# Optimization experiments

Measured on AMD Instinct MI355X. Metric: run time of the kernel, lower is better.

The kernel has to match this reference:

```python
import jax, jax.numpy as jnp
import numpy as np

B, N, D_IN, D_OUT = 4, 2048, 1024, 1024


def setup_inputs() -> dict:
    key = jax.random.key(0)
    k0, k1, k2, k3 = jax.random.split(key, 4)
    x = jax.random.normal(k0, (B, N, D_IN), dtype=jnp.float32)
    # torch Linear weight is [out, in]; store transposed [in, out] for x @ W
    W_query = jax.random.normal(k1, (D_IN, D_OUT), dtype=jnp.float32) * (D_IN ** -0.5)
    W_key = jax.random.normal(k2, (D_IN, D_OUT), dtype=jnp.float32) * (D_IN ** -0.5)
    W_value = jax.random.normal(k3, (D_IN, D_OUT), dtype=jnp.float32) * (D_IN ** -0.5)
    return {"x": x, "W_query": W_query, "W_key": W_key, "W_value": W_value}


def reference(x, W_query, W_key, W_value):
    # x: [B, N, D_IN]
    num_tokens = x.shape[1]
    embed_dim = x.shape[2]  # NB: original scales by INPUT embed dim
    q = jnp.einsum('bnd,de->bne', x, W_query)  # [B, N, D_OUT]
    k = jnp.einsum('bnd,de->bne', x, W_key)
    v = jnp.einsum('bnd,de->bne', x, W_value)
    scores = jnp.einsum('bqe,bke->bqk', q, k)  # [B, N, N]
    idx = jnp.arange(num_tokens)
    causal_mask = idx[None, :] > idx[:, None]  # True above diagonal
    scores = jnp.where(causal_mask[None, :, :], -jnp.inf, scores)
    scale = jnp.asarray(embed_dim, scores.dtype) ** 0.5
    attn = jax.nn.softmax(scores / scale, axis=-1)  # dropout p=0 (eval)
    context = jnp.einsum('bqk,bke->bqe', attn, v)  # [B, N, D_OUT]
    return context
```

## Files before the change

kernel.cpp:

```cpp
#include <hip/hip_runtime.h>


typedef __attribute__((ext_vector_type(8))) _Float16 half8;
typedef __attribute__((ext_vector_type(4))) _Float16 half4v;
typedef __attribute__((ext_vector_type(4))) float floatx4;

#define AS1 __attribute__((address_space(1)))
#define AS3 __attribute__((address_space(3)))

__device__ __forceinline__ void load16_lds(void* lds, const void* g) {
  __builtin_amdgcn_global_load_lds((AS1 void*)g, (AS3 void*)lds, 16, 0, 0);
}

__global__ __launch_bounds__(256)
void prep(const float* __restrict__ in, _Float16* __restrict__ out,
          const float* __restrict__ W0, const float* __restrict__ W1,
          const float* __restrict__ W2, _Float16* __restrict__ Wt) {
  const int bid = blockIdx.x;
  if (bid < 8192) {
    const int i = (bid * 256 + threadIdx.x) << 2;
    float4 v = *(const float4*)(in + i);
    half4v o = { (_Float16)v.x, (_Float16)v.y, (_Float16)v.z, (_Float16)v.w };
    *(half4v*)(out + i) = o;
  } else {
    const int t = bid - 8192;
    const int bz = t >> 10;
    const int rem = t & 1023;
    const int bx = rem & 31, by = rem >> 5;
    const float* W = bz == 0 ? W0 : (bz == 1 ? W1 : W2);
    _Float16* o = Wt + (long long)bz * 1048576;
    __shared__ _Float16 tl[32][33];
    const int tx = threadIdx.x & 31, ty = threadIdx.x >> 5;
    const int n0 = bx << 5, k0 = by << 5;
#pragma unroll
    for (int i = 0; i < 4; ++i)
      tl[ty + i * 8][tx] = (_Float16)W[(long long)(k0 + ty + i * 8) * 1024 + n0 + tx];
    __syncthreads();
#pragma unroll
    for (int i = 0; i < 4; ++i)
      o[(long long)(n0 + ty + i * 8) * 1024 + k0 + tx] = tl[tx][ty + i * 8];
  }
}

__global__ __launch_bounds__(256)
void gemm_qkv(const _Float16* __restrict__ A, const _Float16* __restrict__ B,
              _Float16* __restrict__ Q, _Float16* __restrict__ Kh,
              _Float16* __restrict__ Vt) {
  const int bm = blockIdx.y, bn = blockIdx.x;
  const _Float16* Ab = A + (long long)bm * 128 * 1024;
  const _Float16* Bb = B + (long long)bn * 128 * 1024;

  __shared__ _Float16 As[128][64];
  __shared__ _Float16 Bs[128][64];

  const int tid = threadIdx.x;
  const int wave = tid >> 6, lane = tid & 63;
  const int quad = lane >> 4, lr = lane & 15;
  const int wm = (wave >> 1) << 6, wn = (wave & 1) << 6;
  const int srow = lane >> 3;
  const int goff = ((lane & 7) ^ srow) << 3;

  floatx4 acc[4][4] = {};
  const _Float16* ga = Ab + (long long)(wave * 8 + srow) * 1024 + goff;
  const _Float16* gb = Bb + (long long)(wave * 8 + srow) * 1024 + goff;

  for (int k0 = 0; k0 < 1024; k0 += 64) {
    __syncthreads();
#pragma unroll
    for (int c = 0; c < 4; ++c) {
      load16_lds(&As[wave * 8 + 32 * c][0], ga + c * 32 * 1024);
      load16_lds(&Bs[wave * 8 + 32 * c][0], gb + c * 32 * 1024);
    }
    ga += 64; gb += 64;
    __syncthreads();

#pragma unroll
    for (int kk = 0; kk < 2; ++kk) {
      half8 af[4], bf[4];
#pragma unroll
      for (int i = 0; i < 4; ++i) {
        const int ra = wm + (i << 4) + lr;
        const int rb = wn + (i << 4) + lr;
        af[i] = *(const half8*)&As[ra][(((kk << 2) + quad) ^ (ra & 7)) << 3];
        bf[i] = *(const half8*)&Bs[rb][(((kk << 2) + quad) ^ (rb & 7)) << 3];
      }
#pragma unroll
      for (int i = 0; i < 4; ++i)
#pragma unroll
        for (int j = 0; j < 4; ++j)
          acc[i][j] = __builtin_amdgcn_mfma_f32_16x16x32_f16(af[i], bf[j], acc[i][j], 0, 0, 0);
    }
  }

  const int colb = bn * 128 + wn + lr;
  const int rowb = bm * 128 + wm + (quad << 2);

  if (bn < 16) {
    _Float16* C = (bn < 8) ? Q : Kh;
    const int cb = colb & 1023;
#pragma unroll
    for (int i = 0; i < 4; ++i)
#pragma unroll
      for (int j = 0; j < 4; ++j)
#pragma unroll
        for (int r = 0; r < 4; ++r)
          C[(long long)(rowb + (i << 4) + r) * 1024 + cb + (j << 4)] =
              (_Float16)acc[i][j][r];
  } else {
    const int b = rowb >> 11;
    const int tb = rowb & 2047;
#pragma unroll
    for (int i = 0; i < 4; ++i) {
      const int tok = tb + (i << 4);
#pragma unroll
      for (int j = 0; j < 4; ++j) {
        const int d = (colb & 1023) + (j << 4);
        half4v v = { (_Float16)acc[i][j][0], (_Float16)acc[i][j][1],
                     (_Float16)acc[i][j][2], (_Float16)acc[i][j][3] };
        *(half4v*)&Vt[(long long)b * 2097152 + (long long)d * 2048 + tok] = v;
      }
    }
  }
}

__global__ __launch_bounds__(256)
void gemm_s_exp(const _Float16* __restrict__ Q, const _Float16* __restrict__ Kh,
                _Float16* __restrict__ P, float* __restrict__ M,
                float* __restrict__ L) {
  int t = (blockIdx.x & 7) * 34 + (blockIdx.x >> 3);
  int bn = 0;
  for (;;) { const int c = 32 - 2 * bn; if (t < c) break; t -= c; ++bn; }
  const int qm = 2 * bn + t;
  const int bz = blockIdx.y;

  const _Float16* Ab = Q  + (long long)bz * 2097152 + (long long)qm * 64 * 1024;
  const _Float16* Bb = Kh + (long long)bz * 2097152 + (long long)bn * 128 * 1024;

  __shared__ _Float16 As[64][64];
  __shared__ _Float16 Bs[128][64];
  __shared__ float sm_m[2][2][32];
  __shared__ float sm_s[2][2][32];

  const int tid = threadIdx.x;
  const int wave = tid >> 6, lane = tid & 63;
  const int quad = lane >> 4, lr = lane & 15;
  const int wm1 = wave >> 1, wn1 = wave & 1;
  const int wm = wm1 << 5, wn = wn1 << 6;
  const int srow = lane >> 3;
  const int schunk = lane & 7;
  const int goff = (schunk ^ srow) << 3;

  floatx4 acc[2][4] = {};
  const _Float16* ga = Ab + (long long)(wave * 8 + srow) * 1024 + goff;
  const _Float16* gb = Bb + (long long)(wave * 8 + srow) * 1024 + goff;

  half8 pa[2], pb[4];
#pragma unroll
  for (int c = 0; c < 2; ++c) pa[c] = *(const half8*)(ga + c * 32 * 1024);
#pragma unroll
  for (int c = 0; c < 4; ++c) pb[c] = *(const half8*)(gb + c * 32 * 1024);

  for (int it = 0; it < 16; ++it) {
    __syncthreads();
#pragma unroll
    for (int c = 0; c < 2; ++c)
      *(half8*)&As[wave * 8 + 32 * c + srow][schunk << 3] = pa[c];
#pragma unroll
    for (int c = 0; c < 4; ++c)
      *(half8*)&Bs[wave * 8 + 32 * c + srow][schunk << 3] = pb[c];
    __syncthreads();
    if (it + 1 < 16) {
      const int k1 = (it + 1) << 6;
#pragma unroll
      for (int c = 0; c < 2; ++c)
        pa[c] = *(const half8*)(ga + c * 32 * 1024 + k1);
#pragma unroll
      for (int c = 0; c < 4; ++c)
        pb[c] = *(const half8*)(gb + c * 32 * 1024 + k1);
    }

#pragma unroll
    for (int kk = 0; kk < 2; ++kk) {
      half8 af[2], bf[4];
#pragma unroll
      for (int i = 0; i < 2; ++i) {
        const int ra = wm + (i << 4) + lr;
        af[i] = *(const half8*)&As[ra][(((kk << 2) + quad) ^ (ra & 7)) << 3];
      }
#pragma unroll
      for (int j = 0; j < 4; ++j) {
        const int rb = wn + (j << 4) + lr;
        bf[j] = *(const half8*)&Bs[rb][(((kk << 2) + quad) ^ (rb & 7)) << 3];
      }
#pragma unroll
      for (int i = 0; i < 2; ++i)
#pragma unroll
        for (int j = 0; j < 4; ++j)
          acc[i][j] = __builtin_amdgcn_mfma_f32_16x16x32_f16(af[i], bf[j], acc[i][j], 0, 0, 0);
    }
  }

  const int colb = bn * 128 + wn + lr;
  const int rowb = qm * 64 + wm + (quad << 2);
  _Float16* Pb = P + (long long)bz * 4194304;
  const float scl = 0.03125f;

  float mx[2][4], rs[2][4];
#pragma unroll
  for (int i = 0; i < 2; ++i)
#pragma unroll
    for (int r = 0; r < 4; ++r) { mx[i][r] = -3.0e38f; rs[i][r] = 0.f; }

#pragma unroll
  for (int i = 0; i < 2; ++i)
#pragma unroll
    for (int j = 0; j < 4; ++j)
#pragma unroll
      for (int r = 0; r < 4; ++r) {
        const int qr = rowb + (i << 4) + r;
        const int kcol = colb + (j << 4);
        if (kcol <= qr) mx[i][r] = fmaxf(mx[i][r], acc[i][j][r] * scl);
      }
#pragma unroll
  for (int i = 0; i < 2; ++i)
#pragma unroll
    for (int r = 0; r < 4; ++r) {
#pragma unroll
      for (int off = 1; off < 16; off <<= 1)
        mx[i][r] = fmaxf(mx[i][r], __shfl_xor(mx[i][r], off));
    }

  if (lr == 0) {
#pragma unroll
    for (int i = 0; i < 2; ++i)
#pragma unroll
      for (int r = 0; r < 4; ++r)
        sm_m[wm1][wn1][(i << 4) + (quad << 2) + r] = mx[i][r];
  }
  __syncthreads();
  float mt[2][4];
#pragma unroll
  for (int i = 0; i < 2; ++i)
#pragma unroll
    for (int r = 0; r < 4; ++r)
      mt[i][r] = fmaxf(mx[i][r], sm_m[wm1][wn1 ^ 1][(i << 4) + (quad << 2) + r]);

#pragma unroll
  for (int i = 0; i < 2; ++i)
#pragma unroll
    for (int j = 0; j < 4; ++j)
#pragma unroll
      for (int r = 0; r < 4; ++r) {
        const int qr = rowb + (i << 4) + r;
        const int kcol = colb + (j << 4);
        const float pv =
            (kcol <= qr) ? __expf(acc[i][j][r] * scl - mt[i][r]) : 0.f;
        Pb[(long long)qr * 2048 + kcol] = (_Float16)pv;
        rs[i][r] += pv;
      }

#pragma unroll
  for (int i = 0; i < 2; ++i)
#pragma unroll
    for (int r = 0; r < 4; ++r) {
#pragma unroll
      for (int off = 1; off < 16; off <<= 1)
        rs[i][r] += __shfl_xor(rs[i][r], off);
    }

  if (lr == 0) {
#pragma unroll
    for (int i = 0; i < 2; ++i)
#pragma unroll
      for (int r = 0; r < 4; ++r)
        sm_s[wm1][wn1][(i << 4) + (quad << 2) + r] = rs[i][r];
  }
  __syncthreads();
  if (wn1 == 0 && lr == 0) {
    float* Mb = M + ((long long)bz * 16 + bn) * 2048;
    float* Lb = L + ((long long)bz * 16 + bn) * 2048;
#pragma unroll
    for (int i = 0; i < 2; ++i)
#pragma unroll
      for (int r = 0; r < 4; ++r) {
        const int lrow = (i << 4) + (quad << 2) + r;
        const int row = rowb + (i << 4) + r;
        Mb[row] = mt[i][r];
        Lb[row] = rs[i][r] + sm_s[wm1][1][lrow];
      }
  }
}

__global__ __launch_bounds__(256)
void gemm_pv(const _Float16* __restrict__ P, const _Float16* __restrict__ Vt,
             const float* __restrict__ M, const float* __restrict__ L,
             float* __restrict__ out) {
  const int lid = blockIdx.x + (blockIdx.y << 3) + (blockIdx.z << 7);
  const int xcd = lid & 7;
  const int s = lid >> 3;
  const int p = s >> 4;
  const int dnl = (s >> 2) & 3;
  const int bz = s & 3;
  const int bmg = xcd >> 1, dng = xcd & 1;
  const int bm = (p < 2) ? (15 - 2 * bmg - p) : (2 * bmg + (3 - p));
  const int dn = dng * 4 + dnl;
  const int niter = 2 * (bm + 1);

  const _Float16* Ab = Vt + (long long)bz * 2097152 + (long long)dn * 128 * 2048;
  const _Float16* Bb = P  + (long long)bz * 4194304 + (long long)bm * 128 * 2048;

  __shared__ _Float16 As[128][64];
  __shared__ _Float16 Bs[128][64];
  __shared__ float F_lds[16][128];
  __shared__ float linv_lds[128];

  const int tid = threadIdx.x;
  const int wave = tid >> 6, lane = tid & 63;
  const int quad = lane >> 4, lr = lane & 15;
  const int wm = (wave >> 1) << 6, wn = (wave & 1) << 6;
  const int srow = lane >> 3;
  const int schunk = lane & 7;
  const int goff = (schunk ^ srow) << 3;
  const int lrow0 = wave * 8 + srow;

  if (tid < 128) {
    const float* Mb = M + (long long)bz * 32768 + bm * 128 + tid;
    const float* Lb = L + (long long)bz * 32768 + bm * 128 + tid;
    float mg = -3.0e38f;
    for (int t = 0; t <= bm; ++t) mg = fmaxf(mg, Mb[t * 2048]);
    float ssum = 0.f;
    for (int t = 0; t <= bm; ++t) {
      const float f = __expf(Mb[t * 2048] - mg);
      F_lds[t][tid] = f;
      ssum += f * Lb[t * 2048];
    }
    linv_lds[tid] = 1.0f / ssum;
  }

  floatx4 acc[4][4] = {};
  const _Float16* ga = Ab + (long long)lrow0 * 2048 + goff;
  const _Float16* gb = Bb + (long long)lrow0 * 2048 + goff;

  half8 pa[4], pb[4];
#pragma unroll
  for (int c = 0; c < 4; ++c) {
    pa[c] = *(const half8*)(ga + (long long)c * 32 * 2048);
    pb[c] = *(const half8*)(gb + (long long)c * 32 * 2048);
  }

  for (int it = 0; it < niter; ++it) {
    __syncthreads();
    const int kt = it >> 1;
#pragma unroll
    for (int c = 0; c < 4; ++c) {
      *(half8*)&As[wave * 8 + 32 * c + srow][schunk << 3] = pa[c];
      *(half8*)&Bs[wave * 8 + 32 * c + srow][schunk << 3] =
          pb[c] * (_Float16)F_lds[kt][lrow0 + 32 * c];
    }
    __syncthreads();
    if (it + 1 < niter) {
      const int k1 = (it + 1) << 6;
#pragma unroll
      for (int c = 0; c < 4; ++c) {
        pa[c] = *(const half8*)(ga + (long long)c * 32 * 2048 + k1);
        pb[c] = *(const half8*)(gb + (long long)c * 32 * 2048 + k1);
      }
    }

#pragma unroll
    for (int kk = 0; kk < 2; ++kk) {
      half8 af[4], bf[4];
#pragma unroll
      for (int i = 0; i < 4; ++i) {
        const int ra = wm + (i << 4) + lr;
        const int rb = wn + (i << 4) + lr;
        af[i] = *(const half8*)&As[ra][(((kk << 2) + quad) ^ (ra & 7)) << 3];
        bf[i] = *(const half8*)&Bs[rb][(((kk << 2) + quad) ^ (rb & 7)) << 3];
      }
#pragma unroll
      for (int i = 0; i < 4; ++i)
#pragma unroll
        for (int j = 0; j < 4; ++j)
          acc[i][j] = __builtin_amdgcn_mfma_f32_16x16x32_f16(af[i], bf[j], acc[i][j], 0, 0, 0);
    }
  }

  float* Cb = out + (long long)bz * 2097152;
  const int d0 = dn * 128 + wm + (quad << 2);
  const int q0 = bm * 128 + wn + lr;

  float linv[4];
#pragma unroll
  for (int j = 0; j < 4; ++j) linv[j] = linv_lds[wn + (j << 4) + lr];

#pragma unroll
  for (int i = 0; i < 4; ++i)
#pragma unroll
    for (int j = 0; j < 4; ++j) {
      float4 v = { acc[i][j][0] * linv[j], acc[i][j][1] * linv[j],
                   acc[i][j][2] * linv[j], acc[i][j][3] * linv[j] };
      *(float4*)&Cb[(long long)(q0 + (j << 4)) * 1024 + d0 + (i << 4)] = v;
    }
}


extern "C" void kernel_launch(void* const* d_in, const int* in_sizes, int n_in,
                              void* d_out, int out_size, void* d_ws, size_t ws_size,
                              hipStream_t stream) {
  const float* x  = (const float*)d_in[0];
  const float* Wq = (const float*)d_in[1];
  const float* Wk = (const float*)d_in[2];
  const float* Wv = (const float*)d_in[3];
  float* out = (float*)d_out;

  char* ws = (char*)d_ws;
  _Float16* xh = (_Float16*)(ws);
  _Float16* Wt = (_Float16*)(ws + 16777216);
  _Float16* Q  = (_Float16*)(ws + 23068672);
  _Float16* Kh = (_Float16*)(ws + 39845888);
  _Float16* Vt = (_Float16*)(ws + 56623104);
  _Float16* P  = (_Float16*)(ws + 73400320);
  float*    M  = (float*)   (ws + 106954752);
  float*    L  = (float*)   (ws + 107479040);

  prep<<<11264, 256, 0, stream>>>(x, xh, Wq, Wk, Wv, Wt);

  gemm_qkv<<<dim3(24, 64), 256, 0, stream>>>(xh, Wt, Q, Kh, Vt);

  gemm_s_exp<<<dim3(272, 4), 256, 0, stream>>>(Q, Kh, P, M, L);

  gemm_pv<<<dim3(8, 16, 4), 256, 0, stream>>>(P, Vt, M, L, out);
}
```

Baseline: 229.7 us.

## Fuse fp32-to-fp16 conversion of x into the QKV GEMM operand load

Drops the separate pass that converted x to fp16 in the workspace; the weight transpose now runs as its own kernel. gemm_qkv instead reads fp32 x directly into registers, converts it to fp16 and stores it swizzled into LDS. The next k-tile is prefetched into registers after the barrier so the loads overlap the MFMA work. This removes a full write and re-read of the fp16 copy of x, but each column block now reads fp32 x (twice the bytes), and the prefetch buffers add register pressure.

```diff
diff --git a/kernel.cpp b/kernel.cpp
--- a/kernel.cpp
+++ b/kernel.cpp
@@ -13,41 +13,28 @@
 }
 
 __global__ __launch_bounds__(256)
-void prep(const float* __restrict__ in, _Float16* __restrict__ out,
-          const float* __restrict__ W0, const float* __restrict__ W1,
-          const float* __restrict__ W2, _Float16* __restrict__ Wt) {
-  const int bid = blockIdx.x;
-  if (bid < 8192) {
-    const int i = (bid * 256 + threadIdx.x) << 2;
-    float4 v = *(const float4*)(in + i);
-    half4v o = { (_Float16)v.x, (_Float16)v.y, (_Float16)v.z, (_Float16)v.w };
-    *(half4v*)(out + i) = o;
-  } else {
-    const int t = bid - 8192;
-    const int bz = t >> 10;
-    const int rem = t & 1023;
-    const int bx = rem & 31, by = rem >> 5;
-    const float* W = bz == 0 ? W0 : (bz == 1 ? W1 : W2);
-    _Float16* o = Wt + (long long)bz * 1048576;
-    __shared__ _Float16 tl[32][33];
-    const int tx = threadIdx.x & 31, ty = threadIdx.x >> 5;
-    const int n0 = bx << 5, k0 = by << 5;
-#pragma unroll
-    for (int i = 0; i < 4; ++i)
-      tl[ty + i * 8][tx] = (_Float16)W[(long long)(k0 + ty + i * 8) * 1024 + n0 + tx];
-    __syncthreads();
-#pragma unroll
-    for (int i = 0; i < 4; ++i)
-      o[(long long)(n0 + ty + i * 8) * 1024 + k0 + tx] = tl[tx][ty + i * 8];
-  }
+void transpose_w(const float* __restrict__ W0, const float* __restrict__ W1,
+                 const float* __restrict__ W2, _Float16* __restrict__ Wt) {
+  const float* W = blockIdx.z == 0 ? W0 : (blockIdx.z == 1 ? W1 : W2);
+  _Float16* out = Wt + (long long)blockIdx.z * 1048576;
+  __shared__ _Float16 t[32][33];
+  const int tx = threadIdx.x, ty = threadIdx.y;
+  const int n0 = blockIdx.x << 5, k0 = blockIdx.y << 5;
+#pragma unroll
+  for (int i = 0; i < 4; ++i)
+    t[ty + i * 8][tx] = (_Float16)W[(long long)(k0 + ty + i * 8) * 1024 + n0 + tx];
+  __syncthreads();
+#pragma unroll
+  for (int i = 0; i < 4; ++i)
+    out[(long long)(n0 + ty + i * 8) * 1024 + k0 + tx] = t[tx][ty + i * 8];
 }
 
 __global__ __launch_bounds__(256)
-void gemm_qkv(const _Float16* __restrict__ A, const _Float16* __restrict__ B,
+void gemm_qkv(const float* __restrict__ X, const _Float16* __restrict__ B,
               _Float16* __restrict__ Q, _Float16* __restrict__ Kh,
               _Float16* __restrict__ Vt) {
   const int bm = blockIdx.y, bn = blockIdx.x;
-  const _Float16* Ab = A + (long long)bm * 128 * 1024;
+  const float*    Ab = X + (long long)bm * 128 * 1024;
   const _Float16* Bb = B + (long long)bn * 128 * 1024;
 
   __shared__ _Float16 As[128][64];
@@ -58,21 +45,41 @@
   const int quad = lane >> 4, lr = lane & 15;
   const int wm = (wave >> 1) << 6, wn = (wave & 1) << 6;
   const int srow = lane >> 3;
-  const int goff = ((lane & 7) ^ srow) << 3;
+  const int schunk = lane & 7;
+  const int goff = (schunk ^ srow) << 3;
 
   floatx4 acc[4][4] = {};
-  const _Float16* ga = Ab + (long long)(wave * 8 + srow) * 1024 + goff;
-  const _Float16* gb = Bb + (long long)(wave * 8 + srow) * 1024 + goff;
+  const float*    gax = Ab + (long long)(wave * 8 + srow) * 1024 + goff;
+  const _Float16* gb  = Bb + (long long)(wave * 8 + srow) * 1024 + goff;
+
+  float4 pa0[4], pa1[4];
+#pragma unroll
+  for (int c = 0; c < 4; ++c) {
+    pa0[c] = *(const float4*)(gax + c * 32 * 1024);
+    pa1[c] = *(const float4*)(gax + c * 32 * 1024 + 4);
+  }
 
   for (int k0 = 0; k0 < 1024; k0 += 64) {
     __syncthreads();
 #pragma unroll
     for (int c = 0; c < 4; ++c) {
-      load16_lds(&As[wave * 8 + 32 * c][0], ga + c * 32 * 1024);
+      half8 h = { (_Float16)pa0[c].x, (_Float16)pa0[c].y,
+                  (_Float16)pa0[c].z, (_Float16)pa0[c].w,
+                  (_Float16)pa1[c].x, (_Float16)pa1[c].y,
+                  (_Float16)pa1[c].z, (_Float16)pa1[c].w };
+      *(half8*)&As[wave * 8 + 32 * c + srow][schunk << 3] = h;
       load16_lds(&Bs[wave * 8 + 32 * c][0], gb + c * 32 * 1024);
     }
-    ga += 64; gb += 64;
-    __syncthreads();
+    gb += 64;
+    __syncthreads();
+    if (k0 + 64 < 1024) {
+      const int k1 = k0 + 64;
+#pragma unroll
+      for (int c = 0; c < 4; ++c) {
+        pa0[c] = *(const float4*)(gax + c * 32 * 1024 + k1);
+        pa1[c] = *(const float4*)(gax + c * 32 * 1024 + k1 + 4);
+      }
+    }
 
 #pragma unroll
     for (int kk = 0; kk < 2; ++kk) {
@@ -414,7 +421,6 @@
   float* out = (float*)d_out;
 
   char* ws = (char*)d_ws;
-  _Float16* xh = (_Float16*)(ws);
   _Float16* Wt = (_Float16*)(ws + 16777216);
   _Float16* Q  = (_Float16*)(ws + 23068672);
   _Float16* Kh = (_Float16*)(ws + 39845888);
@@ -423,9 +429,9 @@
   float*    M  = (float*)   (ws + 106954752);
   float*    L  = (float*)   (ws + 107479040);
 
-  prep<<<11264, 256, 0, stream>>>(x, xh, Wq, Wk, Wv, Wt);
-
-  gemm_qkv<<<dim3(24, 64), 256, 0, stream>>>(xh, Wt, Q, Kh, Vt);
+  transpose_w<<<dim3(32, 32, 3), dim3(32, 8), 0, stream>>>(Wq, Wk, Wv, Wt);
+
+  gemm_qkv<<<dim3(24, 64), 256, 0, stream>>>(x, Wt, Q, Kh, Vt);
 
   gemm_s_exp<<<dim3(272, 4), 256, 0, stream>>>(Q, Kh, P, M, L);
 
```

After: 256.4 us. +11.6%, slower.
